# Kernel tuning notes

Measured on AMD Instinct MI355X. Metric: run time of the kernel, lower is better.

## Reference

```python
import jax, jax.numpy as jnp
import numpy as np

N_NODES = 100000
N_EDGES = 1600000
D_IN = 128
D_OUT = 5


def setup_inputs() -> dict:
    key = jax.random.key(0)
    k1, k2, k3, k4, k5 = jax.random.split(key, 5)
    x = jax.random.normal(k1, (N_NODES, D_IN), dtype=jnp.float32)
    edge_index = jax.random.randint(k2, (2, N_EDGES), 0, N_NODES, dtype=jnp.int64)
    scale = 1.0 / np.sqrt(D_IN)
    W_l = jax.random.normal(k3, (D_OUT, D_IN), dtype=jnp.float32) * scale
    b_l = jax.random.normal(k4, (D_OUT,), dtype=jnp.float32) * scale
    W_r = jax.random.normal(k5, (D_OUT, D_IN), dtype=jnp.float32) * scale
    return {"x": x, "edge_index": edge_index, "W_l": W_l, "b_l": b_l, "W_r": W_r}


def reference(x, edge_index, W_l, b_l, W_r):
    # PyG SAGEConv with aggr='mean', root_weight=True:
    # out_i = mean_{j: (j->i) in E} x_j @ W_l^T + b_l + x_i @ W_r^T
    n = x.shape[0]
    src = edge_index[0]
    dst = edge_index[1]
    msgs = x[src]  # [E, D_in] gather (irregular access)
    agg_sum = jax.ops.segment_sum(msgs, dst, num_segments=n)  # [N, D_in]
    deg = jax.ops.segment_sum(jnp.ones(src.shape, dtype=x.dtype), dst, num_segments=n)
    agg_mean = agg_sum / jnp.maximum(deg, 1.0)[:, None]  # zero-degree nodes -> 0
    out = agg_mean @ W_l.T + b_l + x @ W_r.T  # [N, D_out]
    return out
```

## Files before the change

### kernel.cpp

```cpp
#include <hip/hip_runtime.h>
#include <hip/hip_fp16.h>


#define N_NODES 100000
#define N_EDGES 1600000
#define D_IN 128

#define HR_STRIDE 8
#define N_PAD 100352

#define B_NODES 196
#define N_BUCKETS 512
#define CAP 3840

#define SC_EPT 16
#define SC_EPB (256 * SC_EPT)
#define SC_GRID ((N_EDGES + SC_EPB - 1) / SC_EPB)

#define PROJ_NPB 128
#define PROJ_BLOCKS ((N_NODES + PROJ_NPB - 1) / PROJ_NPB)
#define FUSED_GRID (PROJ_BLOCKS + SC_GRID)

typedef unsigned long long u64;
typedef unsigned int u32;

__device__ __forceinline__ float dot8(const float4 a0, const float4 a1,
                                      const float4 b0, const float4 b1) {
    return a0.x * b0.x + a0.y * b0.y + a0.z * b0.z + a0.w * b0.w
         + a1.x * b1.x + a1.y * b1.y + a1.z * b1.z + a1.w * b1.w;
}

__global__ __launch_bounds__(256, 4) void proj_scatter_kernel(
    const float* __restrict__ x,
    const float* __restrict__ Wl,
    const float* __restrict__ Wr,
    uint4* __restrict__ hl,
    float* __restrict__ hr,
    const int* __restrict__ ei,
    u32* __restrict__ sorted,
    int* __restrict__ cursor)
{
    const int tid = threadIdx.x;
    const int m   = blockIdx.x % 3;
    const int d   = blockIdx.x / 3;

    if (m < 2) {
        const int pidx = d * 2 + m;
        const int g = tid >> 4;
        const int k = tid & 15;
        const int node0 = pidx * PROJ_NPB + g * 8;

#pragma unroll
        for (int hb = 0; hb < 2; ++hb) {
            const int nb = node0 + hb * 4;

            float4 xv[4][2];
            int nodes[4];
#pragma unroll
            for (int it = 0; it < 4; ++it) {
                nodes[it] = min(nb + it, N_NODES - 1);
                const float4* xr =
                    (const float4*)(x + (size_t)nodes[it] * D_IN + k * 8);
                xv[it][0] = xr[0];
                xv[it][1] = xr[1];
            }

            {
                float4 wv[5][2];
#pragma unroll
                for (int o = 0; o < 5; ++o) {
                    const float* w = Wl + o * D_IN + k * 8;
                    wv[o][0] = ((const float4*)w)[0];
                    wv[o][1] = ((const float4*)w)[1];
                }
#pragma unroll
                for (int it = 0; it < 4; ++it) {
                    float s[5];
#pragma unroll
                    for (int o = 0; o < 5; ++o)
                        s[o] = dot8(xv[it][0], xv[it][1], wv[o][0], wv[o][1]);
#pragma unroll
                    for (int o = 0; o < 5; ++o) {
                        s[o] += __shfl_xor(s[o], 8, 64);
                        s[o] += __shfl_xor(s[o], 4, 64);
                        s[o] += __shfl_xor(s[o], 2, 64);
                        s[o] += __shfl_xor(s[o], 1, 64);
                    }
                    if (k == 0) {
                        u32 u0 = (u32)__half_as_ushort(__float2half_rn(s[0]));
                        u32 u1 = (u32)__half_as_ushort(__float2half_rn(s[1]));
                        u32 u2 = (u32)__half_as_ushort(__float2half_rn(s[2]));
                        u32 u3 = (u32)__half_as_ushort(__float2half_rn(s[3]));
                        u32 u4 = (u32)__half_as_ushort(__float2half_rn(s[4]));
                        uint4 pk;
                        pk.x = u0 | (u1 << 16);
                        pk.y = u2 | (u3 << 16);
                        pk.z = u4;
                        pk.w = 0u;
                        hl[nodes[it]] = pk;
                    }
                }
            }

            {
                float4 wv[5][2];
#pragma unroll
                for (int o = 0; o < 5; ++o) {
                    const float* w = Wr + o * D_IN + k * 8;
                    wv[o][0] = ((const float4*)w)[0];
                    wv[o][1] = ((const float4*)w)[1];
                }
#pragma unroll
                for (int it = 0; it < 4; ++it) {
                    float s[5];
#pragma unroll
                    for (int o = 0; o < 5; ++o)
                        s[o] = dot8(xv[it][0], xv[it][1], wv[o][0], wv[o][1]);
#pragma unroll
                    for (int o = 0; o < 5; ++o) {
                        s[o] += __shfl_xor(s[o], 8, 64);
                        s[o] += __shfl_xor(s[o], 4, 64);
                        s[o] += __shfl_xor(s[o], 2, 64);
                        s[o] += __shfl_xor(s[o], 1, 64);
                    }
                    if (k == 0) {
                        float* pr = hr + (size_t)nodes[it] * HR_STRIDE;
                        *(float4*)pr = make_float4(s[0], s[1], s[2], s[3]);
                        pr[4] = s[4];
                    }
                }
            }
        }
    } else {
        __shared__ int hist[N_BUCKETS];
        __shared__ int basepos[N_BUCKETS];

        for (int i = tid; i < N_BUCKETS; i += 256) hist[i] = 0;
        __syncthreads();

        const int e0 = d * SC_EPB + tid * SC_EPT;

        int srcv[SC_EPT], dstv[SC_EPT], slot[SC_EPT];
        bool valid[SC_EPT];

        if (e0 + SC_EPT <= N_EDGES) {
            const int4* s4 = (const int4*)(ei + e0);
            const int4* d4 = (const int4*)(ei + N_EDGES + e0);
#pragma unroll
            for (int c = 0; c < SC_EPT / 4; ++c) {
                int4 sv = s4[c], dv = d4[c];
                srcv[c*4+0] = sv.x; srcv[c*4+1] = sv.y;
                srcv[c*4+2] = sv.z; srcv[c*4+3] = sv.w;
                dstv[c*4+0] = dv.x; dstv[c*4+1] = dv.y;
                dstv[c*4+2] = dv.z; dstv[c*4+3] = dv.w;
            }
#pragma unroll
            for (int q = 0; q < SC_EPT; ++q) valid[q] = true;
        } else {
#pragma unroll
            for (int q = 0; q < SC_EPT; ++q) {
                int e = e0 + q;
                valid[q] = (e < N_EDGES);
                srcv[q] = valid[q] ? ei[e] : 0;
                dstv[q] = valid[q] ? ei[N_EDGES + e] : 0;
            }
        }

#pragma unroll
        for (int q = 0; q < SC_EPT; ++q) {
            if (valid[q]) {
                unsigned b = (unsigned)dstv[q] / 196u;
                slot[q] = atomicAdd(&hist[b], 1);
            }
        }
        __syncthreads();

        for (int b = tid; b < N_BUCKETS; b += 256) {
            int c = hist[b];
            if (c > 0) basepos[b] = atomicAdd(&cursor[b], c);
        }
        __syncthreads();

#pragma unroll
        for (int q = 0; q < SC_EPT; ++q) {
            if (valid[q]) {
                unsigned b = (unsigned)dstv[q] / 196u;
                unsigned r = (unsigned)dstv[q] - b * 196u;
                sorted[(size_t)b * CAP + basepos[b] + slot[q]] =
                    (r << 17) | (unsigned)srcv[q];
            }
        }
    }
}

#define AGG_T 512

__global__ __launch_bounds__(512) void agg_kernel(
    const u32* __restrict__ sorted,
    const int* __restrict__ cursor,
    const uint4* __restrict__ hl,
    const float* __restrict__ hr,
    const float* __restrict__ bias,
    float* __restrict__ out)
{
    __shared__ u32 hist[B_NODES];
    __shared__ u32 deg[B_NODES];
    __shared__ u32 offs[B_NODES];
    __shared__ u32 srcs[CAP];
    __shared__ float part[B_NODES][5];

    const int b   = blockIdx.x;
    const int tid = threadIdx.x;

    for (int i = tid; i < B_NODES; i += AGG_T) hist[i] = 0u;
    __syncthreads();

    const int cnt = min(cursor[b], CAP);
    const u32* sp = sorted + (size_t)b * CAP;

    u32 ev[8];
    int rv[8], sl[8];
#pragma unroll
    for (int q = 0; q < 8; ++q) {
        int i = tid + q * AGG_T;
        ev[q] = (i < cnt) ? sp[i] : 0xFFFFFFFFu;
    }
#pragma unroll
    for (int q = 0; q < 8; ++q) {
        if (ev[q] != 0xFFFFFFFFu) {
            rv[q] = (int)(ev[q] >> 17);
            sl[q] = (int)atomicAdd(&hist[rv[q]], 1u);
        }
    }
    __syncthreads();

    if (tid < B_NODES) { deg[tid] = hist[tid]; offs[tid] = hist[tid]; }
    __syncthreads();
#pragma unroll
    for (int s = 1; s < B_NODES; s <<= 1) {
        u32 v = 0;
        if (tid < B_NODES && tid >= s) v = offs[tid - s];
        __syncthreads();
        if (tid < B_NODES) offs[tid] += v;
        __syncthreads();
    }
    if (tid < B_NODES) offs[tid] -= deg[tid];
    __syncthreads();

#pragma unroll
    for (int q = 0; q < 8; ++q) {
        if (ev[q] != 0xFFFFFFFFu)
            srcs[offs[rv[q]] + (u32)sl[q]] = ev[q] & 0x1FFFFu;
    }
    __syncthreads();

    float a0 = 0.f, a1 = 0.f, a2 = 0.f, a3 = 0.f, a4 = 0.f;
    if (tid < 2 * B_NODES) {
        const int p = (tid >= B_NODES);
        const int n = p ? tid - B_NODES : tid;
        const u32 d = deg[n];
        const u32 o = offs[n];
        const u32 h0 = (d + 1) >> 1;
        const u32 i0 = p ? o + h0 : o;
        const u32 i1 = p ? o + d : o + h0;
        for (u32 i = i0; i < i1; ++i) {
            u32 s = srcs[i];
            uint4 h = hl[s];
            a0 += __half2float(__ushort_as_half((unsigned short)(h.x & 0xFFFFu)));
            a1 += __half2float(__ushort_as_half((unsigned short)(h.x >> 16)));
            a2 += __half2float(__ushort_as_half((unsigned short)(h.y & 0xFFFFu)));
            a3 += __half2float(__ushort_as_half((unsigned short)(h.y >> 16)));
            a4 += __half2float(__ushort_as_half((unsigned short)(h.z & 0xFFFFu)));
        }
        if (p) {
            part[n][0] = a0; part[n][1] = a1; part[n][2] = a2;
            part[n][3] = a3; part[n][4] = a4;
        }
    }
    __syncthreads();

    if (tid < B_NODES) {
        const int node = b * B_NODES + tid;
        if (node < N_NODES) {
            a0 += part[tid][0]; a1 += part[tid][1]; a2 += part[tid][2];
            a3 += part[tid][3]; a4 += part[tid][4];
            const float rec = 1.0f / fmaxf((float)deg[tid], 1.0f);
            const float* h = hr + (size_t)node * HR_STRIDE;
            float* o = out + (size_t)node * 5;
            o[0] = a0 * rec + bias[0] + h[0];
            o[1] = a1 * rec + bias[1] + h[1];
            o[2] = a2 * rec + bias[2] + h[2];
            o[3] = a3 * rec + bias[3] + h[3];
            o[4] = a4 * rec + bias[4] + h[4];
        }
    }
}

extern "C" void kernel_launch(void* const* d_in, const int* in_sizes, int n_in,
                              void* d_out, int out_size, void* d_ws, size_t ws_size,
                              hipStream_t stream) {
    const float* x    = (const float*)d_in[0];
    const int*   ei   = (const int*)d_in[1];
    const float* Wl   = (const float*)d_in[2];
    const float* bl   = (const float*)d_in[3];
    const float* Wr   = (const float*)d_in[4];
    float*       out  = (float*)d_out;

    uint4* hl     = (uint4*)d_ws;
    float* hr     = (float*)(hl + N_PAD);
    u32*   sorted = (u32*)(hr + (size_t)N_PAD * HR_STRIDE);
    int*   cursor = (int*)(sorted + (size_t)N_BUCKETS * CAP);

    hipMemsetAsync(cursor, 0, N_BUCKETS * sizeof(int), stream);

    proj_scatter_kernel<<<FUSED_GRID, 256, 0, stream>>>(
        x, Wl, Wr, hl, hr, ei, sorted, cursor);

    agg_kernel<<<N_BUCKETS, 512, 0, stream>>>(sorted, cursor, hl, hr, bl, out);
}
```

Before: 131.8 us.

## Replace bucketed two-level sort with per-node fixed-capacity slots and global atomics

The scatter phase now assigns each edge a slot by a global atomicAdd on a per-node counter and writes it into a fixed 64-entry slot array per node. This drops the shared-memory histogram and bucket pass. The aggregation kernel loses its in-block counting sort and prefix scan, and instead uses four threads per node reading that node's slot list directly, reduced with shuffles. The trade is 1.6M contended global atomics, scattered writes, a larger memset and cursor array, and a capped degree: nodes with more than 64 in-edges are truncated and the mean comes out wrong, though random inputs with average degree 16 are unlikely to reach that.

Measured after the change: 186.0 us. +41.2%, slower.

```diff
diff --git a/kernel.cpp b/kernel.cpp
--- a/kernel.cpp
+++ b/kernel.cpp
@@ -9,9 +9,8 @@
 #define HR_STRIDE 8
 #define N_PAD 100352
 
-#define B_NODES 196
-#define N_BUCKETS 512
-#define CAP 3840
+#define CAP_NODE 64
+#define CAP_SHIFT 6
 
 #define SC_EPT 16
 #define SC_EPB (256 * SC_EPT)
@@ -20,6 +19,9 @@
 #define PROJ_NPB 128
 #define PROJ_BLOCKS ((N_NODES + PROJ_NPB - 1) / PROJ_NPB)
 #define FUSED_GRID (PROJ_BLOCKS + SC_GRID)
+
+#define AGG_NPB 64
+#define AGG_BLOCKS ((N_NODES + AGG_NPB - 1) / AGG_NPB)
 
 typedef unsigned long long u64;
 typedef unsigned int u32;
@@ -132,15 +134,9 @@
             }
         }
     } else {
-        __shared__ int hist[N_BUCKETS];
-        __shared__ int basepos[N_BUCKETS];
-
-        for (int i = tid; i < N_BUCKETS; i += 256) hist[i] = 0;
-        __syncthreads();
-
         const int e0 = d * SC_EPB + tid * SC_EPT;
 
-        int srcv[SC_EPT], dstv[SC_EPT], slot[SC_EPT];
+        int srcv[SC_EPT], dstv[SC_EPT];
         bool valid[SC_EPT];
 
         if (e0 + SC_EPT <= N_EDGES) {
@@ -169,33 +165,16 @@
 #pragma unroll
         for (int q = 0; q < SC_EPT; ++q) {
             if (valid[q]) {
-                unsigned b = (unsigned)dstv[q] / 196u;
-                slot[q] = atomicAdd(&hist[b], 1);
-            }
-        }
-        __syncthreads();
-
-        for (int b = tid; b < N_BUCKETS; b += 256) {
-            int c = hist[b];
-            if (c > 0) basepos[b] = atomicAdd(&cursor[b], c);
-        }
-        __syncthreads();
-
-#pragma unroll
-        for (int q = 0; q < SC_EPT; ++q) {
-            if (valid[q]) {
-                unsigned b = (unsigned)dstv[q] / 196u;
-                unsigned r = (unsigned)dstv[q] - b * 196u;
-                sorted[(size_t)b * CAP + basepos[b] + slot[q]] =
-                    (r << 17) | (unsigned)srcv[q];
+                int slot = atomicAdd(&cursor[dstv[q]], 1);
+                if (slot < CAP_NODE)
+                    sorted[((size_t)dstv[q] << CAP_SHIFT) + slot] =
+                        (u32)srcv[q];
             }
         }
     }
 }
 
-#define AGG_T 512
-
-__global__ __launch_bounds__(512) void agg_kernel(
+__global__ __launch_bounds__(256) void agg_kernel(
     const u32* __restrict__ sorted,
     const int* __restrict__ cursor,
     const uint4* __restrict__ hl,
@@ -203,96 +182,42 @@
     const float* __restrict__ bias,
     float* __restrict__ out)
 {
-    __shared__ u32 hist[B_NODES];
-    __shared__ u32 deg[B_NODES];
-    __shared__ u32 offs[B_NODES];
-    __shared__ u32 srcs[CAP];
-    __shared__ float part[B_NODES][5];
-
-    const int b   = blockIdx.x;
-    const int tid = threadIdx.x;
-
-    for (int i = tid; i < B_NODES; i += AGG_T) hist[i] = 0u;
-    __syncthreads();
-
-    const int cnt = min(cursor[b], CAP);
-    const u32* sp = sorted + (size_t)b * CAP;
-
-    u32 ev[8];
-    int rv[8], sl[8];
-#pragma unroll
-    for (int q = 0; q < 8; ++q) {
-        int i = tid + q * AGG_T;
-        ev[q] = (i < cnt) ? sp[i] : 0xFFFFFFFFu;
+    const int tid  = threadIdx.x;
+    const int sub  = tid & 3;
+    const int nl   = tid >> 2;
+    const int node = blockIdx.x * AGG_NPB + nl;
+    if (node >= N_NODES) return;
+
+    const u32 degf = (u32)cursor[node];
+    const u32 deg  = min(degf, (u32)CAP_NODE);
+    const u32* seg = sorted + ((size_t)node << CAP_SHIFT);
+
+    float a0 = 0.f, a1 = 0.f, a2 = 0.f, a3 = 0.f, a4 = 0.f;
+    for (u32 i = sub; i < deg; i += 4) {
+        u32 s = seg[i];
+        uint4 h = hl[s];
+        a0 += __half2float(__ushort_as_half((unsigned short)(h.x & 0xFFFFu)));
+        a1 += __half2float(__ushort_as_half((unsigned short)(h.x >> 16)));
+        a2 += __half2float(__ushort_as_half((unsigned short)(h.y & 0xFFFFu)));
+        a3 += __half2float(__ushort_as_half((unsigned short)(h.y >> 16)));
+        a4 += __half2float(__ushort_as_half((unsigned short)(h.z & 0xFFFFu)));
     }
-#pragma unroll
-    for (int q = 0; q < 8; ++q) {
-        if (ev[q] != 0xFFFFFFFFu) {
-            rv[q] = (int)(ev[q] >> 17);
-            sl[q] = (int)atomicAdd(&hist[rv[q]], 1u);
-        }
-    }
-    __syncthreads();
-
-    if (tid < B_NODES) { deg[tid] = hist[tid]; offs[tid] = hist[tid]; }
-    __syncthreads();
-#pragma unroll
-    for (int s = 1; s < B_NODES; s <<= 1) {
-        u32 v = 0;
-        if (tid < B_NODES && tid >= s) v = offs[tid - s];
-        __syncthreads();
-        if (tid < B_NODES) offs[tid] += v;
-        __syncthreads();
-    }
-    if (tid < B_NODES) offs[tid] -= deg[tid];
-    __syncthreads();
-
-#pragma unroll
-    for (int q = 0; q < 8; ++q) {
-        if (ev[q] != 0xFFFFFFFFu)
-            srcs[offs[rv[q]] + (u32)sl[q]] = ev[q] & 0x1FFFFu;
-    }
-    __syncthreads();
-
-    float a0 = 0.f, a1 = 0.f, a2 = 0.f, a3 = 0.f, a4 = 0.f;
-    if (tid < 2 * B_NODES) {
-        const int p = (tid >= B_NODES);
-        const int n = p ? tid - B_NODES : tid;
-        const u32 d = deg[n];
-        const u32 o = offs[n];
-        const u32 h0 = (d + 1) >> 1;
-        const u32 i0 = p ? o + h0 : o;
-        const u32 i1 = p ? o + d : o + h0;
-        for (u32 i = i0; i < i1; ++i) {
-            u32 s = srcs[i];
-            uint4 h = hl[s];
-            a0 += __half2float(__ushort_as_half((unsigned short)(h.x & 0xFFFFu)));
-            a1 += __half2float(__ushort_as_half((unsigned short)(h.x >> 16)));
-            a2 += __half2float(__ushort_as_half((unsigned short)(h.y & 0xFFFFu)));
-            a3 += __half2float(__ushort_as_half((unsigned short)(h.y >> 16)));
-            a4 += __half2float(__ushort_as_half((unsigned short)(h.z & 0xFFFFu)));
-        }
-        if (p) {
-            part[n][0] = a0; part[n][1] = a1; part[n][2] = a2;
-            part[n][3] = a3; part[n][4] = a4;
-        }
-    }
-    __syncthreads();
-
-    if (tid < B_NODES) {
-        const int node = b * B_NODES + tid;
-        if (node < N_NODES) {
-            a0 += part[tid][0]; a1 += part[tid][1]; a2 += part[tid][2];
-            a3 += part[tid][3]; a4 += part[tid][4];
-            const float rec = 1.0f / fmaxf((float)deg[tid], 1.0f);
-            const float* h = hr + (size_t)node * HR_STRIDE;
-            float* o = out + (size_t)node * 5;
-            o[0] = a0 * rec + bias[0] + h[0];
-            o[1] = a1 * rec + bias[1] + h[1];
-            o[2] = a2 * rec + bias[2] + h[2];
-            o[3] = a3 * rec + bias[3] + h[3];
-            o[4] = a4 * rec + bias[4] + h[4];
-        }
+
+    a0 += __shfl_xor(a0, 1, 64); a0 += __shfl_xor(a0, 2, 64);
+    a1 += __shfl_xor(a1, 1, 64); a1 += __shfl_xor(a1, 2, 64);
+    a2 += __shfl_xor(a2, 1, 64); a2 += __shfl_xor(a2, 2, 64);
+    a3 += __shfl_xor(a3, 1, 64); a3 += __shfl_xor(a3, 2, 64);
+    a4 += __shfl_xor(a4, 1, 64); a4 += __shfl_xor(a4, 2, 64);
+
+    if (sub == 0) {
+        const float rec = 1.0f / fmaxf((float)deg, 1.0f);
+        const float* h = hr + (size_t)node * HR_STRIDE;
+        float* o = out + (size_t)node * 5;
+        o[0] = a0 * rec + bias[0] + h[0];
+        o[1] = a1 * rec + bias[1] + h[1];
+        o[2] = a2 * rec + bias[2] + h[2];
+        o[3] = a3 * rec + bias[3] + h[3];
+        o[4] = a4 * rec + bias[4] + h[4];
     }
 }
 
@@ -309,12 +234,12 @@
     uint4* hl     = (uint4*)d_ws;
     float* hr     = (float*)(hl + N_PAD);
     u32*   sorted = (u32*)(hr + (size_t)N_PAD * HR_STRIDE);
-    int*   cursor = (int*)(sorted + (size_t)N_BUCKETS * CAP);
-
-    hipMemsetAsync(cursor, 0, N_BUCKETS * sizeof(int), stream);
+    int*   cursor = (int*)(sorted + ((size_t)N_PAD << CAP_SHIFT));
+
+    hipMemsetAsync(cursor, 0, N_PAD * sizeof(int), stream);
 
     proj_scatter_kernel<<<FUSED_GRID, 256, 0, stream>>>(
         x, Wl, Wr, hl, hr, ei, sorted, cursor);
 
-    agg_kernel<<<N_BUCKETS, 512, 0, stream>>>(sorted, cursor, hl, hr, bl, out);
-}
+    agg_kernel<<<AGG_BLOCKS, 256, 0, stream>>>(sorted, cursor, hl, hr, bl, out);
+}
```
